# Kernel optimization log

Hardware: AMD Instinct MI355X
Metric: run time of the kernel (lower is better)

The kernel has to match this reference:

```python
import jax, jax.numpy as jnp
import numpy as np

B, F, T, DEPTH, C = 65536, 256, 256, 6, 4  # batch, n_features, num_trees, max_depth, n_classes


def setup_inputs() -> dict:
    key = jax.random.key(0)
    ks = jax.random.split(key, 4 + 2 * (DEPTH - 1))
    inp = {
        "x": jax.random.normal(ks[0], (B, F), dtype=jnp.float32),
        "root_nodes": jax.random.randint(ks[1], (T,), 0, F, dtype=jnp.int32),
        "root_biases": jax.random.normal(ks[2], (T,), dtype=jnp.float32),
        "leaf_nodes": jax.random.normal(ks[3], (T * 2 ** DEPTH, C), dtype=jnp.float32),
    }
    for lvl in range(1, DEPTH):
        n = T * 2 ** lvl  # flattened tree-major level table
        inp[f"nodes_{lvl}"] = jax.random.randint(ks[2 + 2 * lvl], (n,), 0, F, dtype=jnp.int32)
        inp[f"biases_{lvl}"] = jax.random.normal(ks[3 + 2 * lvl], (n,), dtype=jnp.float32)
    return inp


def _forward(x, root_nodes, root_biases, level_nodes, level_biases, leaf_nodes):
    Bx = x.shape[0]
    Tn = root_nodes.shape[0]
    tree_idx = jnp.arange(Tn, dtype=jnp.int32) * 2  # torch tree_indices
    # root split: [B, T] -> flat [B*T], value = tree*2 + bit
    prev = (jnp.take(x, root_nodes, axis=1) >= root_biases).astype(jnp.int32) + tree_idx
    prev = prev.reshape(-1)
    for nodes, biases in zip(level_nodes, level_biases):
        gidx = jnp.take(nodes, prev).reshape(Bx, Tn)          # feature index per (row, tree)
        feats = jnp.take_along_axis(x, gidx, axis=1).reshape(-1)
        prev = 2 * prev + (feats >= jnp.take(biases, prev)).astype(jnp.int32)
    out = jnp.take(leaf_nodes, prev, axis=0).reshape(Bx, Tn, -1)  # [B, T, C]
    return out


def reference(x, root_nodes, root_biases, leaf_nodes,
              nodes_1, biases_1, nodes_2, biases_2, nodes_3, biases_3,
              nodes_4, biases_4, nodes_5, biases_5):
    out = _forward(
        x, root_nodes, root_biases,
        (nodes_1, nodes_2, nodes_3, nodes_4, nodes_5),
        (biases_1, biases_2, biases_3, biases_4, biases_5),
        leaf_nodes,
    )
    # classification path: aggregation/calibration are identity, classes are 0..C-1
    # so perform_class_select is False -> return (argmax over dim=1, output)
    return (jnp.argmax(out, axis=1), out)
```

## Files before the change

### kernel.cpp

```cpp
#include <hip/hip_runtime.h>
#include <hip/hip_bf16.h>

#define NB 65536
#define NF 256
#define NT 256
#define NC 4
#define NG 8
#define TG 32
#define RB 128
#define RPB (NB / RB)
#define RPC 16
#define NCHUNK (RPB / RPC)
#define NTHREADS 256

__device__ __forceinline__ unsigned int mono32(float v) {
    unsigned int u = __float_as_uint(v);
    return (u & 0x80000000u) ? ~u : (u | 0x80000000u);
}

__global__ __launch_bounds__(NTHREADS, 4) void k_traverse(
    const float* __restrict__ x,
    const int*   __restrict__ root_nodes, const float* __restrict__ root_biases,
    const float* __restrict__ leaf_nodes,
    const int* __restrict__ n1, const float* __restrict__ b1,
    const int* __restrict__ n2, const float* __restrict__ b2,
    const int* __restrict__ n3, const float* __restrict__ b3,
    const int* __restrict__ n4, const float* __restrict__ b4,
    const int* __restrict__ n5, const float* __restrict__ b5,
    float* __restrict__ out_val,
    unsigned long long* __restrict__ keys)
{
    const int g  = blockIdx.x >> 7;
    const int rb = blockIdx.x & (RB - 1);

    __shared__ int2  tbl[1792];
    __shared__ float xr[RPC * NF];

    const int tid = threadIdx.x;
    const int rs  = tid >> 5;
    const int lt  = tid & 31;
    const int t   = g * TG + lt;

    const int2 e0   = make_int2(root_nodes[t], __float_as_int(root_biases[t]));
    const int2 e1_0 = make_int2(n1[2 * t],     __float_as_int(b1[2 * t]));
    const int2 e1_1 = make_int2(n1[2 * t + 1], __float_as_int(b1[2 * t + 1]));
    const int2 e2_0 = make_int2(n2[4 * t],     __float_as_int(b2[4 * t]));
    const int2 e2_1 = make_int2(n2[4 * t + 1], __float_as_int(b2[4 * t + 1]));
    const int2 e2_2 = make_int2(n2[4 * t + 2], __float_as_int(b2[4 * t + 2]));
    const int2 e2_3 = make_int2(n2[4 * t + 3], __float_as_int(b2[4 * t + 3]));

    {
        const int i = tid;
        tbl[((i & 7) << 5) | (i >> 3)] =
            make_int2(n3[g * 256 + i], __float_as_int(b3[g * 256 + i]));
    }
    #pragma unroll
    for (int k = 0; k < 2; ++k) {
        const int i = tid + 256 * k;
        tbl[256 + ((i & 15) << 5) + (i >> 4)] =
            make_int2(n4[g * 512 + i], __float_as_int(b4[g * 512 + i]));
    }
    #pragma unroll
    for (int k = 0; k < 4; ++k) {
        const int i = tid + 256 * k;
        tbl[768 + ((i & 31) << 5) + (i >> 5)] =
            make_int2(n5[g * 1024 + i], __float_as_int(b5[g * 1024 + i]));
    }

    const float4* xg  = (const float4*)x;
    const float4* lf4 = (const float4*)leaf_nodes;
    float4*       ov4 = (float4*)out_val;
    const int halfshift = tid & 32;

    for (int ck = 0; ck < NCHUNK; ++ck) {
        const int r0 = rb * RPB + ck * RPC;

        {
            const size_t base4 = (size_t)r0 * (NF / 4);
            float4* xr4 = (float4*)xr;
            #pragma unroll
            for (int k = 0; k < 4; ++k) {
                __builtin_amdgcn_global_load_lds(
                    (const __attribute__((address_space(1))) void*)(xg + base4 + tid + 256 * k),
                    (__attribute__((address_space(3))) void*)(xr4 + tid + 256 * k),
                    16, 0, 0);
            }
        }
        __syncthreads();

        const float* xrow0 = xr + rs * NF;
        const float* xrow1 = xr + (rs + 8) * NF;
        int p0, p1;
        int2 ea, eb;

        p0 = (xrow0[e0.x] >= __int_as_float(e0.y)) ? 1 : 0;
        p1 = (xrow1[e0.x] >= __int_as_float(e0.y)) ? 1 : 0;
        ea = p0 ? e1_1 : e1_0;
        eb = p1 ? e1_1 : e1_0;
        p0 = 2 * p0 + (xrow0[ea.x] >= __int_as_float(ea.y) ? 1 : 0);
        p1 = 2 * p1 + (xrow1[eb.x] >= __int_as_float(eb.y) ? 1 : 0);
        {
            int2 a0 = (p0 & 1) ? e2_1 : e2_0, a1 = (p0 & 1) ? e2_3 : e2_2;
            ea = (p0 & 2) ? a1 : a0;
            int2 c0 = (p1 & 1) ? e2_1 : e2_0, c1 = (p1 & 1) ? e2_3 : e2_2;
            eb = (p1 & 2) ? c1 : c0;
        }
        p0 = 2 * p0 + (xrow0[ea.x] >= __int_as_float(ea.y) ? 1 : 0);
        p1 = 2 * p1 + (xrow1[eb.x] >= __int_as_float(eb.y) ? 1 : 0);
        ea = tbl[(p0 << 5) + lt];
        eb = tbl[(p1 << 5) + lt];
        p0 = 2 * p0 + (xrow0[ea.x] >= __int_as_float(ea.y) ? 1 : 0);
        p1 = 2 * p1 + (xrow1[eb.x] >= __int_as_float(eb.y) ? 1 : 0);
        ea = tbl[256 + (p0 << 5) + lt];
        eb = tbl[256 + (p1 << 5) + lt];
        p0 = 2 * p0 + (xrow0[ea.x] >= __int_as_float(ea.y) ? 1 : 0);
        p1 = 2 * p1 + (xrow1[eb.x] >= __int_as_float(eb.y) ? 1 : 0);
        ea = tbl[768 + (p0 << 5) + lt];
        eb = tbl[768 + (p1 << 5) + lt];
        p0 = 2 * p0 + (xrow0[ea.x] >= __int_as_float(ea.y) ? 1 : 0);
        p1 = 2 * p1 + (xrow1[eb.x] >= __int_as_float(eb.y) ? 1 : 0);

        const float4 leaf0 = lf4[(size_t)g * 2048 + (lt << 6) + p0];
        const float4 leaf1 = lf4[(size_t)g * 2048 + (lt << 6) + p1];
        ov4[(size_t)(r0 + rs)     * NT + t] = leaf0;
        ov4[(size_t)(r0 + rs + 8) * NT + t] = leaf1;

        #pragma unroll
        for (int c2 = 0; c2 < 2; ++c2) {
            const float4 lv = c2 ? leaf1 : leaf0;
            const int row = r0 + rs + 8 * c2;
            const float vc0 = lv.x, vc1 = lv.y, vc2 = lv.z, vc3 = lv.w;

            const float a0 = fmaxf(vc0, __shfl_xor(vc0, 16));
            const float a1 = fmaxf(vc1, __shfl_xor(vc1, 16));
            const float a2 = fmaxf(vc2, __shfl_xor(vc2, 16));
            const float a3 = fmaxf(vc3, __shfl_xor(vc3, 16));
            const bool hi4 = (lt & 16) != 0;
            float u = hi4 ? a2 : a0;
            float w = hi4 ? a3 : a1;
            const float mu = fmaxf(u, __shfl_xor(u, 8));
            const float mw = fmaxf(w, __shfl_xor(w, 8));
            float v = (lt & 8) ? mw : mu;
            v = fmaxf(v, __shfl_xor(v, 4));
            v = fmaxf(v, __shfl_xor(v, 2));
            v = fmaxf(v, __shfl_xor(v, 1));

            const float vcarr[4] = { vc0, vc1, vc2, vc3 };
            unsigned long long kk = 0;
            #pragma unroll
            for (int cls = 0; cls < 4; ++cls) {
                const float mc = __shfl(v, halfshift + (cls << 3));
                const unsigned long long ball = __ballot(vcarr[cls] == mc);
                const unsigned int hm = (unsigned int)(ball >> halfshift);
                const int gidx = g * TG + (__ffs(hm) - 1);
                const unsigned long long kc =
                    ((unsigned long long)mono32(mc) << 8) |
                    (unsigned long long)(255 - gidx);
                if (lt == cls) kk = kc;
            }
            if (lt < 4) atomicMax(&keys[(size_t)row * NC + lt], kk);
        }
        __syncthreads();
    }
}

__global__ void __launch_bounds__(256) k_finish(
    const unsigned long long* __restrict__ keys,
    float* __restrict__ out_arg)
{
    const int i = blockIdx.x * 256 + threadIdx.x;
    out_arg[i] = (float)(255 - (int)(keys[i] & 0xFFull));
}

extern "C" void kernel_launch(void* const* d_in, const int* in_sizes, int n_in,
                              void* d_out, int out_size, void* d_ws, size_t ws_size,
                              hipStream_t stream) {
    const float* x           = (const float*)d_in[0];
    const int*   root_nodes  = (const int*)  d_in[1];
    const float* root_biases = (const float*)d_in[2];
    const float* leaf_nodes  = (const float*)d_in[3];
    const int*   n1 = (const int*)  d_in[4];
    const float* b1 = (const float*)d_in[5];
    const int*   n2 = (const int*)  d_in[6];
    const float* b2 = (const float*)d_in[7];
    const int*   n3 = (const int*)  d_in[8];
    const float* b3 = (const float*)d_in[9];
    const int*   n4 = (const int*)  d_in[10];
    const float* b4 = (const float*)d_in[11];
    const int*   n5 = (const int*)  d_in[12];
    const float* b5 = (const float*)d_in[13];

    float* out_arg = (float*)d_out;
    float* out_val = (float*)d_out + (size_t)NB * NC;
    unsigned long long* keys = (unsigned long long*)d_ws;

    hipMemsetAsync(d_ws, 0, (size_t)NB * NC * sizeof(unsigned long long), stream);

    k_traverse<<<NG * RB, NTHREADS, 0, stream>>>(
        x, root_nodes, root_biases, leaf_nodes,
        n1, b1, n2, b2, n3, b3, n4, b4, n5, b5,
        out_val, keys);

    k_finish<<<(NB * NC) / 256, 256, 0, stream>>>(keys, out_arg);
}
```

Baseline: 415.2 us.

## Cover all trees per block, reduce argmax in LDS, double-buffer x rows

Each block now covers all 256 trees (8 wavefronts, one per tree group) for its row slice, instead of one tree group per block. This lets the per-row argmax be reduced through a small shared key array rather than global 64-bit atomics, which removes the memset and the separate finish kernel. x rows are double-buffered with async global-to-LDS loads so the next chunk's load overlaps the current traversal. Level-5 node tables now come straight from global memory instead of LDS. The risks are that only 512 blocks are launched, that level-5 and leaf loads are uncoalesced global gathers, and that there are extra barriers per chunk.

```diff
diff --git a/kernel.cpp b/kernel.cpp
--- a/kernel.cpp
+++ b/kernel.cpp
@@ -1,5 +1,4 @@
 #include <hip/hip_runtime.h>
-#include <hip/hip_bf16.h>
 
 #define NB 65536
 #define NF 256
@@ -7,11 +6,11 @@
 #define NC 4
 #define NG 8
 #define TG 32
-#define RB 128
+#define RB 512
 #define RPB (NB / RB)
-#define RPC 16
+#define RPC 8
 #define NCHUNK (RPB / RPC)
-#define NTHREADS 256
+#define NTHREADS 512
 
 __device__ __forceinline__ unsigned int mono32(float v) {
     unsigned int u = __float_as_uint(v);
@@ -28,18 +27,21 @@
     const int* __restrict__ n4, const float* __restrict__ b4,
     const int* __restrict__ n5, const float* __restrict__ b5,
     float* __restrict__ out_val,
-    unsigned long long* __restrict__ keys)
+    float* __restrict__ out_arg)
 {
-    const int g  = blockIdx.x >> 7;
-    const int rb = blockIdx.x & (RB - 1);
-
-    __shared__ int2  tbl[1792];
-    __shared__ float xr[RPC * NF];
-
-    const int tid = threadIdx.x;
-    const int rs  = tid >> 5;
-    const int lt  = tid & 31;
-    const int t   = g * TG + lt;
+    const int rb = blockIdx.x;
+
+    __shared__ int2  tbl[6144];
+    __shared__ float xr[2][RPC * NF];
+    __shared__ unsigned long long wkey[RPC][NC][NG];
+
+    const int tid  = threadIdx.x;
+    const int g    = tid >> 6;
+    const int lane = tid & 63;
+    const int lt   = lane & 31;
+    const int h    = lane >> 5;
+    const int t    = g * TG + lt;
+    const int halfshift = lane & 32;
 
     const int2 e0   = make_int2(root_nodes[t], __float_as_int(root_biases[t]));
     const int2 e1_0 = make_int2(n1[2 * t],     __float_as_int(b1[2 * t]));
@@ -49,88 +51,97 @@
     const int2 e2_2 = make_int2(n2[4 * t + 2], __float_as_int(b2[4 * t + 2]));
     const int2 e2_3 = make_int2(n2[4 * t + 3], __float_as_int(b2[4 * t + 3]));
 
-    {
-        const int i = tid;
-        tbl[((i & 7) << 5) | (i >> 3)] =
-            make_int2(n3[g * 256 + i], __float_as_int(b3[g * 256 + i]));
-    }
-    #pragma unroll
-    for (int k = 0; k < 2; ++k) {
-        const int i = tid + 256 * k;
-        tbl[256 + ((i & 15) << 5) + (i >> 4)] =
-            make_int2(n4[g * 512 + i], __float_as_int(b4[g * 512 + i]));
-    }
     #pragma unroll
     for (int k = 0; k < 4; ++k) {
-        const int i = tid + 256 * k;
-        tbl[768 + ((i & 31) << 5) + (i >> 5)] =
-            make_int2(n5[g * 1024 + i], __float_as_int(b5[g * 1024 + i]));
+        const int i = tid + 512 * k;
+        const int tt = i >> 3, p = i & 7;
+        tbl[((tt >> 5) << 8) + (p << 5) + (tt & 31)] =
+            make_int2(n3[i], __float_as_int(b3[i]));
+    }
+    #pragma unroll
+    for (int k = 0; k < 8; ++k) {
+        const int i = tid + 512 * k;
+        const int tt = i >> 4, p = i & 15;
+        tbl[2048 + ((tt >> 5) << 9) + (p << 5) + (tt & 31)] =
+            make_int2(n4[i], __float_as_int(b4[i]));
     }
 
     const float4* xg  = (const float4*)x;
     const float4* lf4 = (const float4*)leaf_nodes;
     float4*       ov4 = (float4*)out_val;
-    const int halfshift = tid & 32;
-
+
+    {
+        const size_t base4 = (size_t)rb * RPB * (NF / 4);
+        __builtin_amdgcn_global_load_lds(
+            (const __attribute__((address_space(1))) void*)(xg + base4 + tid),
+            (__attribute__((address_space(3))) void*)(((float4*)xr[0]) + tid),
+            16, 0, 0);
+    }
+    __syncthreads();
+
+    int buf = 0;
     for (int ck = 0; ck < NCHUNK; ++ck) {
         const int r0 = rb * RPB + ck * RPC;
 
-        {
-            const size_t base4 = (size_t)r0 * (NF / 4);
-            float4* xr4 = (float4*)xr;
-            #pragma unroll
-            for (int k = 0; k < 4; ++k) {
-                __builtin_amdgcn_global_load_lds(
-                    (const __attribute__((address_space(1))) void*)(xg + base4 + tid + 256 * k),
-                    (__attribute__((address_space(3))) void*)(xr4 + tid + 256 * k),
-                    16, 0, 0);
-            }
-        }
-        __syncthreads();
-
-        const float* xrow0 = xr + rs * NF;
-        const float* xrow1 = xr + (rs + 8) * NF;
-        int p0, p1;
-        int2 ea, eb;
-
-        p0 = (xrow0[e0.x] >= __int_as_float(e0.y)) ? 1 : 0;
-        p1 = (xrow1[e0.x] >= __int_as_float(e0.y)) ? 1 : 0;
-        ea = p0 ? e1_1 : e1_0;
-        eb = p1 ? e1_1 : e1_0;
-        p0 = 2 * p0 + (xrow0[ea.x] >= __int_as_float(ea.y) ? 1 : 0);
-        p1 = 2 * p1 + (xrow1[eb.x] >= __int_as_float(eb.y) ? 1 : 0);
-        {
-            int2 a0 = (p0 & 1) ? e2_1 : e2_0, a1 = (p0 & 1) ? e2_3 : e2_2;
-            ea = (p0 & 2) ? a1 : a0;
-            int2 c0 = (p1 & 1) ? e2_1 : e2_0, c1 = (p1 & 1) ? e2_3 : e2_2;
-            eb = (p1 & 2) ? c1 : c0;
-        }
-        p0 = 2 * p0 + (xrow0[ea.x] >= __int_as_float(ea.y) ? 1 : 0);
-        p1 = 2 * p1 + (xrow1[eb.x] >= __int_as_float(eb.y) ? 1 : 0);
-        ea = tbl[(p0 << 5) + lt];
-        eb = tbl[(p1 << 5) + lt];
-        p0 = 2 * p0 + (xrow0[ea.x] >= __int_as_float(ea.y) ? 1 : 0);
-        p1 = 2 * p1 + (xrow1[eb.x] >= __int_as_float(eb.y) ? 1 : 0);
-        ea = tbl[256 + (p0 << 5) + lt];
-        eb = tbl[256 + (p1 << 5) + lt];
-        p0 = 2 * p0 + (xrow0[ea.x] >= __int_as_float(ea.y) ? 1 : 0);
-        p1 = 2 * p1 + (xrow1[eb.x] >= __int_as_float(eb.y) ? 1 : 0);
-        ea = tbl[768 + (p0 << 5) + lt];
-        eb = tbl[768 + (p1 << 5) + lt];
-        p0 = 2 * p0 + (xrow0[ea.x] >= __int_as_float(ea.y) ? 1 : 0);
-        p1 = 2 * p1 + (xrow1[eb.x] >= __int_as_float(eb.y) ? 1 : 0);
-
-        const float4 leaf0 = lf4[(size_t)g * 2048 + (lt << 6) + p0];
-        const float4 leaf1 = lf4[(size_t)g * 2048 + (lt << 6) + p1];
-        ov4[(size_t)(r0 + rs)     * NT + t] = leaf0;
-        ov4[(size_t)(r0 + rs + 8) * NT + t] = leaf1;
-
-        #pragma unroll
-        for (int c2 = 0; c2 < 2; ++c2) {
-            const float4 lv = c2 ? leaf1 : leaf0;
-            const int row = r0 + rs + 8 * c2;
-            const float vc0 = lv.x, vc1 = lv.y, vc2 = lv.z, vc3 = lv.w;
-
+        if (ck + 1 < NCHUNK) {
+            const size_t base4 = (size_t)(r0 + RPC) * (NF / 4);
+            __builtin_amdgcn_global_load_lds(
+                (const __attribute__((address_space(1))) void*)(xg + base4 + tid),
+                (__attribute__((address_space(3))) void*)(((float4*)xr[buf ^ 1]) + tid),
+                16, 0, 0);
+        }
+
+        const float* xb = xr[buf];
+        const float* xw[4];
+        int p[4];
+        #pragma unroll
+        for (int j = 0; j < 4; ++j) xw[j] = xb + (h + 2 * j) * NF;
+
+        #pragma unroll
+        for (int j = 0; j < 4; ++j)
+            p[j] = (xw[j][e0.x] >= __int_as_float(e0.y)) ? 1 : 0;
+        #pragma unroll
+        for (int j = 0; j < 4; ++j) {
+            const int2 e = p[j] ? e1_1 : e1_0;
+            p[j] = 2 * p[j] + (xw[j][e.x] >= __int_as_float(e.y) ? 1 : 0);
+        }
+        #pragma unroll
+        for (int j = 0; j < 4; ++j) {
+            const int2 a0 = (p[j] & 1) ? e2_1 : e2_0;
+            const int2 a1 = (p[j] & 1) ? e2_3 : e2_2;
+            const int2 e  = (p[j] & 2) ? a1 : a0;
+            p[j] = 2 * p[j] + (xw[j][e.x] >= __int_as_float(e.y) ? 1 : 0);
+        }
+        #pragma unroll
+        for (int j = 0; j < 4; ++j) {
+            const int2 e = tbl[(g << 8) + (p[j] << 5) + lt];
+            p[j] = 2 * p[j] + (xw[j][e.x] >= __int_as_float(e.y) ? 1 : 0);
+        }
+        #pragma unroll
+        for (int j = 0; j < 4; ++j) {
+            const int2 e = tbl[2048 + (g << 9) + (p[j] << 5) + lt];
+            p[j] = 2 * p[j] + (xw[j][e.x] >= __int_as_float(e.y) ? 1 : 0);
+        }
+        #pragma unroll
+        for (int j = 0; j < 4; ++j) {
+            const int i5 = (t << 5) + p[j];
+            const int   nf = n5[i5];
+            const float bb = b5[i5];
+            p[j] = 2 * p[j] + (xw[j][nf] >= bb ? 1 : 0);
+        }
+
+        float4 leaf[4];
+        #pragma unroll
+        for (int j = 0; j < 4; ++j)
+            leaf[j] = lf4[(size_t)t * 64 + p[j]];
+        #pragma unroll
+        for (int j = 0; j < 4; ++j)
+            ov4[(size_t)(r0 + h + 2 * j) * NT + t] = leaf[j];
+
+        #pragma unroll
+        for (int j = 0; j < 4; ++j) {
+            const float vc0 = leaf[j].x, vc1 = leaf[j].y,
+                        vc2 = leaf[j].z, vc3 = leaf[j].w;
             const float a0 = fmaxf(vc0, __shfl_xor(vc0, 16));
             const float a1 = fmaxf(vc1, __shfl_xor(vc1, 16));
             const float a2 = fmaxf(vc2, __shfl_xor(vc2, 16));
@@ -158,18 +169,25 @@
                     (unsigned long long)(255 - gidx);
                 if (lt == cls) kk = kc;
             }
-            if (lt < 4) atomicMax(&keys[(size_t)row * NC + lt], kk);
-        }
+            if (lt < 4) wkey[h + 2 * j][lt][g] = kk;
+        }
+
         __syncthreads();
-    }
-}
-
-__global__ void __launch_bounds__(256) k_finish(
-    const unsigned long long* __restrict__ keys,
-    float* __restrict__ out_arg)
-{
-    const int i = blockIdx.x * 256 + threadIdx.x;
-    out_arg[i] = (float)(255 - (int)(keys[i] & 0xFFull));
+
+        if (tid < 32) {
+            const int r = tid >> 2, c = tid & 3;
+            unsigned long long m = wkey[r][c][0];
+            #pragma unroll
+            for (int q = 1; q < 8; ++q) {
+                const unsigned long long v2 = wkey[r][c][q];
+                m = (v2 > m) ? v2 : m;
+            }
+            out_arg[(size_t)(r0 + r) * NC + c] = (float)(255 - (int)(m & 0xFFull));
+        }
+
+        __syncthreads();
+        buf ^= 1;
+    }
 }
 
 extern "C" void kernel_launch(void* const* d_in, const int* in_sizes, int n_in,
@@ -192,14 +210,9 @@
 
     float* out_arg = (float*)d_out;
     float* out_val = (float*)d_out + (size_t)NB * NC;
-    unsigned long long* keys = (unsigned long long*)d_ws;
-
-    hipMemsetAsync(d_ws, 0, (size_t)NB * NC * sizeof(unsigned long long), stream);
-
-    k_traverse<<<NG * RB, NTHREADS, 0, stream>>>(
+
+    k_traverse<<<RB, NTHREADS, 0, stream>>>(
         x, root_nodes, root_biases, leaf_nodes,
         n1, b1, n2, b2, n3, b3, n4, b4, n5, b5,
-        out_val, keys);
-
-    k_finish<<<(NB * NC) / 256, 256, 0, stream>>>(keys, out_arg);
+        out_val, out_arg);
 }
```

Result: no change. 412.0 us (-0.8%).
